# Kernel tuning notes

Measured on AMD Instinct MI355X. Metric: run time of the kernel, lower is better.

Reference implementation:

```python
import jax, jax.numpy as jnp
import numpy as np

R, T, M, N, L = 128, 4096, 32768, 4096, 16384
ALPHA_LO, ALPHA_HI = 0.01, 1.0
BETA_LO, BETA_HI = 1.0, 8.0


def setup_inputs() -> dict:
    key = jax.random.key(0)
    ks = jax.random.split(key, 7)
    x = jax.random.normal(ks[0], (R, T), dtype=jnp.float32)          # route flows param
    A = jax.random.uniform(ks[1], (M, R), dtype=jnp.float32)          # route->movement incidence
    t0 = jax.random.uniform(ks[2], (L,), dtype=jnp.float32) * 10.0    # free-flow time per c_df row
    cap = jax.random.uniform(ks[3], (L,), dtype=jnp.float32) * 1000.0 + 500.0  # capacity
    radio = jax.random.uniform(ks[4], (L,), dtype=jnp.float32)
    node_ids = jax.random.randint(ks[5], (M,), 0, N, dtype=jnp.int32)  # node of each movement row
    row_node = jax.random.randint(ks[6], (L,), 0, N, dtype=jnp.int32)  # node of each c_df row
    # logit((0.15-0.01)/0.99) and logit((4-1)/7) anchors
    alpha_raw = jnp.float32(np.log(0.141414 / (1 - 0.141414)))
    beta_raw = jnp.float32(np.log((3.0 / 7.0) / (1 - 3.0 / 7.0)))
    return {"x": x, "A": A, "t0": t0, "cap": cap, "radio": radio,
            "alpha_raw": alpha_raw, "beta_raw": beta_raw,
            "node_ids": node_ids, "row_node": row_node}


def reference(x, A, t0, cap, radio, alpha_raw, beta_raw, node_ids, row_node):
    alpha = ALPHA_LO + (ALPHA_HI - ALPHA_LO) * jax.nn.sigmoid(alpha_raw)
    beta = BETA_LO + (BETA_HI - BETA_LO) * jax.nn.sigmoid(beta_raw)
    x_pos = jax.nn.relu(x)                                   # relu(x).clamp(min=0)
    c_pred = A @ x_pos                                        # [M, T]
    # per-node flow: segment-sum of movement rows grouped by node
    node_flow = jax.ops.segment_sum(c_pred, node_ids, num_segments=N)  # [N, T]
    flow = node_flow[row_node]                                # [L, T] gather per c_df row
    ratio = jnp.maximum(flow / cap[:, None], 1e-6)            # (flow/cap).clamp(min=1e-6)
    # y = sum_rows t0*radio + sum_rows t0*alpha*radio * ratio**beta
    y = jnp.sum(t0 * radio) + jnp.einsum("l,lt->t", t0 * alpha * radio, ratio ** beta)
    return (x_pos, c_pred, y)
```

## Files before the change

### kernel.cpp

```cpp
#include <hip/hip_runtime.h>

#define T_DIM 4096
#define R_DIM 128
#define M_DIM 32768
#define N_DIM 4096
#define L_DIM 16384

typedef __attribute__((ext_vector_type(8))) short short8;
typedef __attribute__((ext_vector_type(4))) float float4_;

__device__ __forceinline__ unsigned short f2bf(float f) {
    unsigned int u = __float_as_uint(f);
    unsigned int r = (u + 0x7fffu + ((u >> 16) & 1u)) >> 16;
    return (unsigned short)r;
}

__global__ __launch_bounds__(256) void prep_x(const float* __restrict__ x,
                                              float* __restrict__ xpos,
                                              unsigned short* __restrict__ Xt) {
    int id = blockIdx.x * 256 + threadIdx.x;
    int k = id >> 12;
    int t = id & (T_DIM - 1);
    float v = fmaxf(x[id], 0.0f);
    xpos[id] = v;
    Xt[t * R_DIM + k] = f2bf(v);
}

__global__ __launch_bounds__(256) void cast_A_seg(const float* __restrict__ A,
                                                  const int* __restrict__ node_ids,
                                                  unsigned short* __restrict__ Ab,
                                                  float* __restrict__ Bseg) {
    int id = blockIdx.x * 256 + threadIdx.x;
    int m = id >> 7;
    int k = id & (R_DIM - 1);
    float v = A[id];
    Ab[id] = f2bf(v);
    atomicAdd(Bseg + node_ids[m] * R_DIM + k, v);
}

__global__ __launch_bounds__(256) void cast_Bseg(const float* __restrict__ Bseg,
                                                 unsigned short* __restrict__ Bb) {
    int id = blockIdx.x * 256 + threadIdx.x;
    Bb[id] = f2bf(Bseg[id]);
}

__global__ __launch_bounds__(256) void prep_lw(const float* __restrict__ t0,
                                               const float* __restrict__ cap,
                                               const float* __restrict__ radio,
                                               const float* __restrict__ alpha_raw,
                                               float* __restrict__ w,
                                               float* __restrict__ rcap,
                                               float* __restrict__ cterm) {
    int l = blockIdx.x * 256 + threadIdx.x;
    float alpha = 0.01f + 0.99f / (1.0f + expf(-alpha_raw[0]));
    float tv = t0[l], rv = radio[l];
    w[l] = tv * alpha * rv;
    rcap[l] = 1.0f / cap[l];
    float p = tv * rv;
    #pragma unroll
    for (int off = 32; off > 0; off >>= 1) p += __shfl_down(p, off, 64);
    if ((threadIdx.x & 63) == 0) atomicAdd(cterm, p);
}

__global__ __launch_bounds__(256) void gemm_mfma(const unsigned short* __restrict__ Am,
                                                 const unsigned short* __restrict__ Xt,
                                                 float* __restrict__ C) {
    const int lane = threadIdx.x & 63;
    const int wid  = threadIdx.x >> 6;
    const int quad = lane >> 4;
    const int l16  = lane & 15;
    const int mBase = blockIdx.y * 128 + (wid & 1) * 64;
    const int tBase = blockIdx.x * 128 + (wid >> 1) * 64;

    float4_ acc[4][4];
    #pragma unroll
    for (int i = 0; i < 4; i++)
        #pragma unroll
        for (int j = 0; j < 4; j++)
            acc[i][j] = (float4_)(0.0f);

    #pragma unroll
    for (int ks = 0; ks < 4; ks++) {
        const int k0 = ks * 32 + quad * 8;
        short8 a[4], b[4];
        #pragma unroll
        for (int i = 0; i < 4; i++) {
            size_t m = (size_t)(mBase + i * 16 + l16);
            a[i] = *(const short8*)(Am + m * R_DIM + k0);
        }
        #pragma unroll
        for (int j = 0; j < 4; j++) {
            size_t t = (size_t)(tBase + j * 16 + l16);
            b[j] = *(const short8*)(Xt + t * R_DIM + k0);
        }
        #pragma unroll
        for (int i = 0; i < 4; i++)
            #pragma unroll
            for (int j = 0; j < 4; j++)
                acc[i][j] = __builtin_amdgcn_mfma_f32_16x16x32_bf16(a[i], b[j], acc[i][j], 0, 0, 0);
    }

    #pragma unroll
    for (int i = 0; i < 4; i++) {
        int row0 = mBase + i * 16 + quad * 4;
        #pragma unroll
        for (int j = 0; j < 4; j++) {
            int col = tBase + j * 16 + l16;
            #pragma unroll
            for (int r = 0; r < 4; r++) {
                C[(size_t)(row0 + r) * T_DIM + col] = acc[i][j][r];
            }
        }
    }
}

__global__ __launch_bounds__(256) void stage5(const float* __restrict__ nflow,
                                              const int* __restrict__ row_node,
                                              const float* __restrict__ w,
                                              const float* __restrict__ rcap,
                                              const float* __restrict__ beta_raw,
                                              const float* __restrict__ cterm,
                                              float* __restrict__ y) {
    const int t  = blockIdx.x * 256 + threadIdx.x;
    const int lc = blockIdx.y;
    const int LPC = L_DIM / 32;
    const int l0 = lc * LPC;
    float beta = 1.0f + 7.0f / (1.0f + expf(-beta_raw[0]));
    float acc = 0.0f;
    for (int i = 0; i < LPC; i++) {
        int l = l0 + i;
        int rn = row_node[l];
        float flow = nflow[(size_t)rn * T_DIM + t];
        float ratio = fmaxf(flow * rcap[l], 1e-6f);
        acc += w[l] * __builtin_amdgcn_exp2f(beta * __builtin_amdgcn_logf(ratio));
    }
    if (lc == 0) acc += cterm[0];
    atomicAdd(&y[t], acc);
}

extern "C" void kernel_launch(void* const* d_in, const int* in_sizes, int n_in,
                              void* d_out, int out_size, void* d_ws, size_t ws_size,
                              hipStream_t stream) {
    const float* x         = (const float*)d_in[0];
    const float* A         = (const float*)d_in[1];
    const float* t0        = (const float*)d_in[2];
    const float* cap       = (const float*)d_in[3];
    const float* radio     = (const float*)d_in[4];
    const float* alpha_raw = (const float*)d_in[5];
    const float* beta_raw  = (const float*)d_in[6];
    const int*   node_ids  = (const int*)d_in[7];
    const int*   row_node  = (const int*)d_in[8];

    float* out   = (float*)d_out;
    float* xpos  = out;
    float* cpred = out + (size_t)R_DIM * T_DIM;
    float* y     = cpred + (size_t)M_DIM * T_DIM;

    char* ws = (char*)d_ws;
    unsigned short* Xt   = (unsigned short*)(ws);
    unsigned short* Ab   = (unsigned short*)(ws + (1u << 20));
    unsigned short* Bb   = (unsigned short*)(ws + (9u << 20));
    float*          Bseg = (float*)(ws + (10u << 20));
    float*          w    = (float*)(ws + (12u << 20));
    float*          rcap = (float*)(ws + (12u << 20) + 65536);
    float*          csum = (float*)(ws + (12u << 20) + 131072);
    float*          nflw = (float*)(ws + (16u << 20));

    (void)hipMemsetAsync(Bseg, 0, (size_t)N_DIM * R_DIM * sizeof(float), stream);
    (void)hipMemsetAsync(csum, 0, sizeof(float), stream);
    (void)hipMemsetAsync(y, 0, T_DIM * sizeof(float), stream);

    prep_x    <<<dim3((R_DIM * T_DIM) / 256), 256, 0, stream>>>(x, xpos, Xt);
    cast_A_seg<<<dim3((M_DIM * R_DIM) / 256), 256, 0, stream>>>(A, node_ids, Ab, Bseg);
    cast_Bseg <<<dim3((N_DIM * R_DIM) / 256), 256, 0, stream>>>(Bseg, Bb);
    prep_lw   <<<dim3(L_DIM / 256), 256, 0, stream>>>(t0, cap, radio, alpha_raw, w, rcap, csum);

    gemm_mfma<<<dim3(T_DIM / 128, M_DIM / 128), 256, 0, stream>>>(Ab, Xt, cpred);
    gemm_mfma<<<dim3(T_DIM / 128, N_DIM / 128), 256, 0, stream>>>(Bb, Xt, nflw);

    stage5<<<dim3(T_DIM / 256, 32), 256, 0, stream>>>(nflw, row_node, w, rcap, beta_raw, csum, y);
}
```

Baseline: 721.0 us.

## Fold per-row coefficients into per-node weights and fuse y reduction into nflow GEMM

Rewrites y using (flow/cap)^beta = flow^beta * cap^-beta, so all c_df rows sharing a node collapse into one per-node coefficient built by atomics in prep_lw. The y reduction is then fused into the epilogue of the node-flow GEMM, which removes the node_flow buffer round trip and the separate gather-based stage5 kernel. Other changes ride along: prep_x now transposes through LDS for coalesced stores, the cast kernels use float4 vector accesses, and both GEMMs remap workgroups with an XCD-aware swizzle. The trade-off is that the 1e-6 clamp on the ratio becomes a 1e-30 clamp on flow, which changes behaviour for tiny or negative flows, and that the per-node atomics order changes the floating-point summation order.

Measured after the change: 699.9 us. 1.03x faster.

```diff
diff --git a/kernel.cpp b/kernel.cpp
--- a/kernel.cpp
+++ b/kernel.cpp
@@ -7,6 +7,7 @@
 #define L_DIM 16384
 
 typedef __attribute__((ext_vector_type(8))) short short8;
+typedef __attribute__((ext_vector_type(4))) short short4_;
 typedef __attribute__((ext_vector_type(4))) float float4_;
 
 __device__ __forceinline__ unsigned short f2bf(float f) {
@@ -18,12 +19,27 @@
 __global__ __launch_bounds__(256) void prep_x(const float* __restrict__ x,
                                               float* __restrict__ xpos,
                                               unsigned short* __restrict__ Xt) {
-    int id = blockIdx.x * 256 + threadIdx.x;
-    int k = id >> 12;
-    int t = id & (T_DIM - 1);
-    float v = fmaxf(x[id], 0.0f);
-    xpos[id] = v;
-    Xt[t * R_DIM + k] = f2bf(v);
+    __shared__ unsigned short lds[64][130];
+    const int tid = threadIdx.x;
+    const int t0 = blockIdx.x * 64;
+    #pragma unroll
+    for (int it = 0; it < 32; it++) {
+        int idx = it * 256 + tid;
+        int k = idx >> 6;
+        int tt = idx & 63;
+        float v = fmaxf(x[k * T_DIM + t0 + tt], 0.0f);
+        xpos[k * T_DIM + t0 + tt] = v;
+        lds[tt][k] = f2bf(v);
+    }
+    __syncthreads();
+    const int w = tid >> 6, lane = tid & 63;
+    #pragma unroll
+    for (int rep = 0; rep < 16; rep++) {
+        int row = w * 16 + rep;
+        unsigned int lo = lds[row][2 * lane];
+        unsigned int hi = lds[row][2 * lane + 1];
+        *(unsigned int*)(Xt + (size_t)(t0 + row) * R_DIM + 2 * lane) = lo | (hi << 16);
+    }
 }
 
 __global__ __launch_bounds__(256) void cast_A_seg(const float* __restrict__ A,
@@ -31,46 +47,74 @@
                                                   unsigned short* __restrict__ Ab,
                                                   float* __restrict__ Bseg) {
     int id = blockIdx.x * 256 + threadIdx.x;
-    int m = id >> 7;
-    int k = id & (R_DIM - 1);
-    float v = A[id];
-    Ab[id] = f2bf(v);
-    atomicAdd(Bseg + node_ids[m] * R_DIM + k, v);
+    int m = id >> 5;
+    int k = (id & 31) << 2;
+    float4 v = *(const float4*)(A + (size_t)m * R_DIM + k);
+    short4_ b;
+    b.x = (short)f2bf(v.x); b.y = (short)f2bf(v.y);
+    b.z = (short)f2bf(v.z); b.w = (short)f2bf(v.w);
+    *(short4_*)(Ab + (size_t)m * R_DIM + k) = b;
+    float* dst = Bseg + (size_t)node_ids[m] * R_DIM + k;
+    atomicAdd(dst + 0, v.x);
+    atomicAdd(dst + 1, v.y);
+    atomicAdd(dst + 2, v.z);
+    atomicAdd(dst + 3, v.w);
 }
 
 __global__ __launch_bounds__(256) void cast_Bseg(const float* __restrict__ Bseg,
                                                  unsigned short* __restrict__ Bb) {
     int id = blockIdx.x * 256 + threadIdx.x;
-    Bb[id] = f2bf(Bseg[id]);
+    float4 v = *(const float4*)(Bseg + (size_t)id * 4);
+    short4_ b;
+    b.x = (short)f2bf(v.x); b.y = (short)f2bf(v.y);
+    b.z = (short)f2bf(v.z); b.w = (short)f2bf(v.w);
+    *(short4_*)(Bb + (size_t)id * 4) = b;
 }
 
 __global__ __launch_bounds__(256) void prep_lw(const float* __restrict__ t0,
                                                const float* __restrict__ cap,
                                                const float* __restrict__ radio,
                                                const float* __restrict__ alpha_raw,
-                                               float* __restrict__ w,
-                                               float* __restrict__ rcap,
+                                               const float* __restrict__ beta_raw,
+                                               const int* __restrict__ row_node,
+                                               float* __restrict__ gcoef,
                                                float* __restrict__ cterm) {
     int l = blockIdx.x * 256 + threadIdx.x;
     float alpha = 0.01f + 0.99f / (1.0f + expf(-alpha_raw[0]));
+    float beta  = 1.0f + 7.0f  / (1.0f + expf(-beta_raw[0]));
     float tv = t0[l], rv = radio[l];
-    w[l] = tv * alpha * rv;
-    rcap[l] = 1.0f / cap[l];
+    float rc = 1.0f / cap[l];
+    float wv = tv * alpha * rv;
+    float g = wv * __builtin_amdgcn_exp2f(beta * __builtin_amdgcn_logf(rc));
+    atomicAdd(gcoef + row_node[l], g);
     float p = tv * rv;
     #pragma unroll
     for (int off = 32; off > 0; off >>= 1) p += __shfl_down(p, off, 64);
     if ((threadIdx.x & 63) == 0) atomicAdd(cterm, p);
+}
+
+__global__ __launch_bounds__(256) void y_init(const float* __restrict__ cterm,
+                                              float* __restrict__ y) {
+    int t = blockIdx.x * 256 + threadIdx.x;
+    y[t] = cterm[0];
 }
 
 __global__ __launch_bounds__(256) void gemm_mfma(const unsigned short* __restrict__ Am,
                                                  const unsigned short* __restrict__ Xt,
                                                  float* __restrict__ C) {
+    const int nwg  = gridDim.x * gridDim.y;
+    const int orig = blockIdx.y * gridDim.x + blockIdx.x;
+    const int cpx  = nwg >> 3;
+    const int swz  = (orig & 7) * cpx + (orig >> 3);
+    const int bx   = swz & 31;
+    const int by   = swz >> 5;
+
     const int lane = threadIdx.x & 63;
     const int wid  = threadIdx.x >> 6;
     const int quad = lane >> 4;
     const int l16  = lane & 15;
-    const int mBase = blockIdx.y * 128 + (wid & 1) * 64;
-    const int tBase = blockIdx.x * 128 + (wid >> 1) * 64;
+    const int mBase = by * 128 + (wid & 1) * 64;
+    const int tBase = bx * 128 + (wid >> 1) * 64;
 
     float4_ acc[4][4];
     #pragma unroll
@@ -114,28 +158,80 @@
     }
 }
 
-__global__ __launch_bounds__(256) void stage5(const float* __restrict__ nflow,
-                                              const int* __restrict__ row_node,
-                                              const float* __restrict__ w,
-                                              const float* __restrict__ rcap,
-                                              const float* __restrict__ beta_raw,
-                                              const float* __restrict__ cterm,
-                                              float* __restrict__ y) {
-    const int t  = blockIdx.x * 256 + threadIdx.x;
-    const int lc = blockIdx.y;
-    const int LPC = L_DIM / 32;
-    const int l0 = lc * LPC;
+__global__ __launch_bounds__(256) void gemm_nflow_y(const unsigned short* __restrict__ Bb,
+                                                    const unsigned short* __restrict__ Xt,
+                                                    const float* __restrict__ gcoef,
+                                                    const float* __restrict__ beta_raw,
+                                                    float* __restrict__ y) {
+    const int nwg  = gridDim.x * gridDim.y;
+    const int orig = blockIdx.y * gridDim.x + blockIdx.x;
+    const int cpx  = nwg >> 3;
+    const int swz  = (orig & 7) * cpx + (orig >> 3);
+    const int bx   = swz & 31;
+    const int by   = swz >> 5;
+
+    const int lane = threadIdx.x & 63;
+    const int wid  = threadIdx.x >> 6;
+    const int quad = lane >> 4;
+    const int l16  = lane & 15;
+    const int bRow  = by * 128;
+    const int mBase = bRow + (wid & 1) * 64;
+    const int tBase = bx * 128 + (wid >> 1) * 64;
+
+    __shared__ float gc[128];
+    if (threadIdx.x < 128) gc[threadIdx.x] = gcoef[bRow + threadIdx.x];
+
+    float4_ acc[4][4];
+    #pragma unroll
+    for (int i = 0; i < 4; i++)
+        #pragma unroll
+        for (int j = 0; j < 4; j++)
+            acc[i][j] = (float4_)(0.0f);
+
+    #pragma unroll
+    for (int ks = 0; ks < 4; ks++) {
+        const int k0 = ks * 32 + quad * 8;
+        short8 a[4], b[4];
+        #pragma unroll
+        for (int i = 0; i < 4; i++) {
+            size_t m = (size_t)(mBase + i * 16 + l16);
+            a[i] = *(const short8*)(Bb + m * R_DIM + k0);
+        }
+        #pragma unroll
+        for (int j = 0; j < 4; j++) {
+            size_t t = (size_t)(tBase + j * 16 + l16);
+            b[j] = *(const short8*)(Xt + t * R_DIM + k0);
+        }
+        #pragma unroll
+        for (int i = 0; i < 4; i++)
+            #pragma unroll
+            for (int j = 0; j < 4; j++)
+                acc[i][j] = __builtin_amdgcn_mfma_f32_16x16x32_bf16(a[i], b[j], acc[i][j], 0, 0, 0);
+    }
+
+    __syncthreads();
     float beta = 1.0f + 7.0f / (1.0f + expf(-beta_raw[0]));
-    float acc = 0.0f;
-    for (int i = 0; i < LPC; i++) {
-        int l = l0 + i;
-        int rn = row_node[l];
-        float flow = nflow[(size_t)rn * T_DIM + t];
-        float ratio = fmaxf(flow * rcap[l], 1e-6f);
-        acc += w[l] * __builtin_amdgcn_exp2f(beta * __builtin_amdgcn_logf(ratio));
-    }
-    if (lc == 0) acc += cterm[0];
-    atomicAdd(&y[t], acc);
+    float p[4] = {0.0f, 0.0f, 0.0f, 0.0f};
+    #pragma unroll
+    for (int i = 0; i < 4; i++) {
+        int r0 = (wid & 1) * 64 + i * 16 + quad * 4;
+        #pragma unroll
+        for (int r = 0; r < 4; r++) {
+            float g = gc[r0 + r];
+            #pragma unroll
+            for (int j = 0; j < 4; j++) {
+                float f = acc[i][j][r];
+                float pw = __builtin_amdgcn_exp2f(beta * __builtin_amdgcn_logf(fmaxf(f, 1e-30f)));
+                p[j] += g * pw;
+            }
+        }
+    }
+    #pragma unroll
+    for (int j = 0; j < 4; j++) {
+        p[j] += __shfl_xor(p[j], 16, 64);
+        p[j] += __shfl_xor(p[j], 32, 64);
+        if (quad == 0) atomicAdd(&y[tBase + j * 16 + l16], p[j]);
+    }
 }
 
 extern "C" void kernel_launch(void* const* d_in, const int* in_sizes, int n_in,
@@ -157,26 +253,23 @@
     float* y     = cpred + (size_t)M_DIM * T_DIM;
 
     char* ws = (char*)d_ws;
-    unsigned short* Xt   = (unsigned short*)(ws);
-    unsigned short* Ab   = (unsigned short*)(ws + (1u << 20));
-    unsigned short* Bb   = (unsigned short*)(ws + (9u << 20));
-    float*          Bseg = (float*)(ws + (10u << 20));
-    float*          w    = (float*)(ws + (12u << 20));
-    float*          rcap = (float*)(ws + (12u << 20) + 65536);
-    float*          csum = (float*)(ws + (12u << 20) + 131072);
-    float*          nflw = (float*)(ws + (16u << 20));
+    unsigned short* Xt    = (unsigned short*)(ws);
+    unsigned short* Ab    = (unsigned short*)(ws + (1u << 20));
+    unsigned short* Bb    = (unsigned short*)(ws + (9u << 20));
+    float*          Bseg  = (float*)(ws + (10u << 20));
+    float*          gcoef = (float*)(ws + (12u << 20));
+    float*          csum  = gcoef + N_DIM;
 
     (void)hipMemsetAsync(Bseg, 0, (size_t)N_DIM * R_DIM * sizeof(float), stream);
-    (void)hipMemsetAsync(csum, 0, sizeof(float), stream);
-    (void)hipMemsetAsync(y, 0, T_DIM * sizeof(float), stream);
-
-    prep_x    <<<dim3((R_DIM * T_DIM) / 256), 256, 0, stream>>>(x, xpos, Xt);
-    cast_A_seg<<<dim3((M_DIM * R_DIM) / 256), 256, 0, stream>>>(A, node_ids, Ab, Bseg);
-    cast_Bseg <<<dim3((N_DIM * R_DIM) / 256), 256, 0, stream>>>(Bseg, Bb);
-    prep_lw   <<<dim3(L_DIM / 256), 256, 0, stream>>>(t0, cap, radio, alpha_raw, w, rcap, csum);
+    (void)hipMemsetAsync(gcoef, 0, (size_t)(N_DIM + 1) * sizeof(float), stream);
+
+    prep_x    <<<dim3(T_DIM / 64), 256, 0, stream>>>(x, xpos, Xt);
+    cast_A_seg<<<dim3((M_DIM * R_DIM / 4) / 256), 256, 0, stream>>>(A, node_ids, Ab, Bseg);
+    cast_Bseg <<<dim3((N_DIM * R_DIM / 4) / 256), 256, 0, stream>>>(Bseg, Bb);
+    prep_lw   <<<dim3(L_DIM / 256), 256, 0, stream>>>(t0, cap, radio, alpha_raw,
+                                                      beta_raw, row_node, gcoef, csum);
+    y_init    <<<dim3(T_DIM / 256), 256, 0, stream>>>(csum, y);
 
     gemm_mfma<<<dim3(T_DIM / 128, M_DIM / 128), 256, 0, stream>>>(Ab, Xt, cpred);
-    gemm_mfma<<<dim3(T_DIM / 128, N_DIM / 128), 256, 0, stream>>>(Bb, Xt, nflw);
-
-    stage5<<<dim3(T_DIM / 256, 32), 256, 0, stream>>>(nflw, row_node, w, rcap, beta_raw, csum, y);
-}
+    gemm_nflow_y<<<dim3(T_DIM / 128, N_DIM / 128), 256, 0, stream>>>(Bb, Xt, gcoef, beta_raw, y);
+}
```
